# Kernel optimization log

Measured on AMD Instinct MI355X. Metric: run time of the kernel, lower is better.

The kernel has to match this reference:

```python
import jax, jax.numpy as jnp
import numpy as np

B, N = 64, 4096          # trees per batch, leaves per complete binary tree
V, S = 21, 50            # amino-acid vocab, grammar-symbol vocab
E, H = 64, 128           # embed_dim, hidden_dim


def setup_inputs() -> dict:
    key = jax.random.key(0)
    ks = jax.random.split(key, 16)

    def lin_w(k, din, dout):
        return (jax.random.normal(k, (dout, din), jnp.float32) / np.sqrt(din)).astype(jnp.float32)

    tokens = jax.random.randint(ks[0], (B, N), 0, V, dtype=jnp.int32)
    symbols = jax.random.randint(ks[1], (B, N - 1), 0, S, dtype=jnp.int32)

    emb = jax.random.normal(ks[2], (V, E), jnp.float32) * 0.02
    emb = emb.at[0].set(0.0)  # padding_idx=0
    sym_emb = jax.random.normal(ks[3], (S, E), jnp.float32) * 0.02

    return {
        "tokens": tokens, "symbols": symbols,
        "emb": emb, "sym_emb": sym_emb,
        "Wp": lin_w(ks[4], E, H), "bp": jnp.zeros((H,), jnp.float32),
        "Wi": lin_w(ks[5], H, H), "bi": jnp.zeros((H,), jnp.float32),
        "Ui": lin_w(ks[6], H, H),
        "Wf": lin_w(ks[7], H, H), "bf": jnp.zeros((H,), jnp.float32),
        "Uf": lin_w(ks[8], H, H),
        "Wo": lin_w(ks[9], H, H), "bo": jnp.zeros((H,), jnp.float32),
        "Uo": lin_w(ks[10], H, H),
        "Wu": lin_w(ks[11], H, H), "bu": jnp.zeros((H,), jnp.float32),
        "Uu": lin_w(ks[12], H, H),
        "Wout": lin_w(ks[13], H, H), "bout": jnp.zeros((H,), jnp.float32),
    }


def _encode(tokens, symbols, emb, sym_emb, Wp, bp, Wi, bi, Ui, Wf, bf, Uf,
            Wo, bo, Uo, Wu, bu, Uu, Wout, bout):
    emb = emb.at[0].set(0.0)  # padding row contributes nothing (and gets no grad)

    # Leaf nodes: amino-acid embedding -> input_proj, no children.
    x = emb[tokens] @ Wp.T + bp                      # [B, N, H]
    i = jax.nn.sigmoid(x @ Wi.T + bi)
    o = jax.nn.sigmoid(x @ Wo.T + bo)
    u = jnp.tanh(x @ Wu.T + bu)
    c = i * u                                        # [B, N, H]
    h = o * jnp.tanh(c)

    # Bottom-up over levels of the complete binary tree (Child-Sum Tree-LSTM).
    off, n = 0, N
    while n > 1:
        m = n // 2
        xs = sym_emb[symbols[:, off:off + m]] @ Wp.T + bp   # [B, m, H]
        hl, hr = h[:, 0::2], h[:, 1::2]
        cl, cr = c[:, 0::2], c[:, 1::2]
        ht = hl + hr                                         # h_tilde = sum_j h_j
        gi = jax.nn.sigmoid(xs @ Wi.T + bi + ht @ Ui.T)
        go = jax.nn.sigmoid(xs @ Wo.T + bo + ht @ Uo.T)
        gu = jnp.tanh(xs @ Wu.T + bu + ht @ Uu.T)
        fx = xs @ Wf.T + bf
        fl = jax.nn.sigmoid(fx + hl @ Uf.T)                  # per-child forget gates
        fr = jax.nn.sigmoid(fx + hr @ Uf.T)
        c = gi * gu + fl * cl + fr * cr
        h = go * jnp.tanh(c)
        off += m
        n = m

    root_h = h[:, 0]                                         # [B, H]
    return root_h @ Wout.T + bout                            # output_proj


def reference(tokens, symbols, emb, sym_emb, Wp, bp, Wi, bi, Ui, Wf, bf, Uf,
              Wo, bo, Uo, Wu, bu, Uu, Wout, bout):
    return _encode(tokens, symbols, emb, sym_emb, Wp, bp, Wi, bi, Ui, Wf, bf,
                   Uf, Wo, bo, Uo, Wu, bu, Uu, Wout, bout)
```

## Files before the change

### kernel.cpp

```cpp
#include <hip/hip_runtime.h>
#include <hip/hip_bf16.h>

typedef __attribute__((ext_vector_type(8))) short short8;
typedef __attribute__((ext_vector_type(4))) float f32x4;

static constexpr int B_ = 64;
static constexpr int N_ = 4096;
static constexpr int V_ = 21;
static constexpr int S_ = 50;
static constexpr int E_ = 64;
static constexpr int H_ = 128;
static constexpr int NPAIR = V_ * V_;
static constexpr int NTAB = NPAIR * S_;

__device__ __forceinline__ float rcp_(float x) { return __builtin_amdgcn_rcpf(x); }
__device__ __forceinline__ float sigm(float x) { return rcp_(1.0f + __expf(-x)); }
__device__ __forceinline__ float tanh_(float x) {
  float a = fabsf(x);
  float e = __expf(-2.0f * a);
  float t = (1.0f - e) * rcp_(1.0f + e);
  return x < 0.0f ? -t : t;
}
__device__ __forceinline__ unsigned short f2bf(float f) {
  __hip_bfloat16 b = __float2bfloat16(f);
  return *reinterpret_cast<unsigned short*>(&b);
}
__device__ __forceinline__ float bf2f(unsigned short u) {
  return __uint_as_float(((unsigned int)u) << 16);
}

struct Gates { float cv, hv; };
__device__ __forceinline__ Gates gate_combine(float4 sx,
    float i_p, float o_p, float u_p, float fl_p, float fr_p, float cl, float cr) {
  float gi = sigm(sx.x + i_p);
  float go = sigm(sx.y + o_p);
  float gu = tanh_(sx.z + u_p);
  float fl = sigm(sx.w + fl_p);
  float fr = sigm(sx.w + fr_p);
  float cv = fmaf(gi, gu, fmaf(fl, cl, fr * cr));
  Gates g; g.cv = cv; g.hv = go * tanh_(cv);
  return g;
}

__global__ void __launch_bounds__(512) k_pre0(
    const float* __restrict__ Ui, const float* __restrict__ Uo,
    const float* __restrict__ Uu, const float* __restrict__ Uf,
    const float* __restrict__ Wi, const float* __restrict__ Wo,
    const float* __restrict__ Wu, const float* __restrict__ Wf,
    const float* __restrict__ Wp, const float* __restrict__ Wout,
    unsigned short* __restrict__ Wfrag, float* __restrict__ Wt,
    float* __restrict__ Wxt, float* __restrict__ Wpt,
    float* __restrict__ Woutt) {
  __shared__ float Tt[32][129];
  int blk = blockIdx.x, t = threadIdx.x;
  if (blk < 16) {
    int idx = blk * 512 + t;
    int L = idx & 63;
    int K = (idx >> 6) & 3;
    int T = idx >> 8;
    int n = 16 * T + (L & 15);
    int k0 = 32 * K + ((L >> 4) << 3);
    int g = n >> 7, o = n & 127;
    const float* U = (g == 0) ? Ui : (g == 1) ? Uo : (g == 2) ? Uu : Uf;
    unsigned short out[8];
    #pragma unroll
    for (int j = 0; j < 8; ++j) out[j] = f2bf(U[o * 128 + k0 + j]);
    *(int4*)(Wfrag + (size_t)idx * 8) = *(int4*)out;
  } else if (blk < 48) {
    int job = blk - 16;
    int m = job >> 2, kt = job & 3;
    int k0 = kt * 32;
    const float* M = (m == 0) ? Ui : (m == 1) ? Uo : (m == 2) ? Uu : (m == 3) ? Uf
                   : (m == 4) ? Wi : (m == 5) ? Wo : (m == 6) ? Wu : Wf;
    float* D = (m < 4) ? Wt : Wxt;
    int g = m & 3;
    #pragma unroll
    for (int pass = 0; pass < 2; ++pass) {
      int o = (t >> 3) + 64 * pass;
      int kk = 4 * (t & 7);
      float4 v = *(const float4*)(M + o * 128 + k0 + kk);
      Tt[kk][o] = v.x; Tt[kk + 1][o] = v.y; Tt[kk + 2][o] = v.z; Tt[kk + 3][o] = v.w;
    }
    __syncthreads();
    #pragma unroll
    for (int pass = 0; pass < 8; ++pass) {
      int kk = pass * 4 + (t >> 7);
      int o = t & 127;
      D[(size_t)(k0 + kk) * 512 + g * 128 + o] = Tt[kk][o];
    }
  } else if (blk == 48) {
    for (int i = t; i < E_ * H_; i += 512) {
      int e = i >> 7, o = i & 127;
      Wpt[i] = Wp[o * E_ + e];
    }
  } else {
    for (int i = t; i < H_ * H_; i += 512) {
      int k = i >> 7, o = i & 127;
      Woutt[i] = Wout[o * H_ + k];
    }
  }
}

__global__ void __launch_bounds__(512) k_pre1(
    const float* __restrict__ emb, const float* __restrict__ sym_emb,
    const float* __restrict__ Wpt, const float* __restrict__ Wxt,
    const float* __restrict__ Wt,
    const float* __restrict__ bp, const float* __restrict__ bi,
    const float* __restrict__ bo, const float* __restrict__ bu,
    const float* __restrict__ bfv,
    unsigned short* __restrict__ leaf_h8, float* __restrict__ leaf_c,
    float* __restrict__ symx, float* __restrict__ P_leaf) {
  __shared__ float x[128];
  __shared__ float zs[512];
  __shared__ float hl[128];
  int blk = blockIdx.x, t = threadIdx.x;
  if (blk < V_) {
    int v = blk;
    if (t < 128) {
      float acc = bp[t];
      if (v != 0) {
        for (int e = 0; e < E_; ++e) acc = fmaf(emb[v * E_ + e], Wpt[e * 128 + t], acc);
      }
      x[t] = acc;
    }
    __syncthreads();
    if (t < 384) {
      int g = t >> 7;
      const float* bb = (g == 0) ? bi : (g == 1) ? bo : bu;
      float z = bb[t & 127];
      for (int k = 0; k < H_; ++k) z = fmaf(x[k], Wxt[k * 512 + t], z);
      zs[t] = z;
    }
    __syncthreads();
    if (t < 128) {
      float gi = sigm(zs[t]), go = sigm(zs[128 + t]), gu = tanh_(zs[256 + t]);
      float c = gi * gu;
      leaf_c[v * H_ + t] = c;
      unsigned short hb = f2bf(go * tanh_(c));
      leaf_h8[v * H_ + t] = hb;
      hl[t] = bf2f(hb);
    }
    __syncthreads();
    {
      float z = 0.f;
      for (int k = 0; k < H_; ++k) z = fmaf(hl[k], Wt[k * 512 + t], z);
      P_leaf[(size_t)v * 512 + t] = z;
    }
  } else {
    int s = blk - V_;
    if (t < 128) {
      float acc = bp[t];
      for (int e = 0; e < E_; ++e) acc = fmaf(sym_emb[s * E_ + e], Wpt[e * 128 + t], acc);
      x[t] = acc;
    }
    __syncthreads();
    {
      int g = t >> 7;
      const float* bb = (g == 0) ? bi : (g == 1) ? bo : (g == 2) ? bu : bfv;
      float z = bb[t & 127];
      for (int k = 0; k < H_; ++k) z = fmaf(x[k], Wxt[k * 512 + t], z);
      zs[t] = z;
    }
    __syncthreads();
    if (t < 128) {
      float4 v4 = make_float4(zs[t], zs[128 + t], zs[256 + t], zs[384 + t]);
      *(float4*)(symx + (size_t)s * 512 + t * 4) = v4;
    }
  }
}

__global__ void k_tabB(const float* __restrict__ P_leaf, const float* __restrict__ symx,
                       const float* __restrict__ leaf_c,
                       const int* __restrict__ tokens, const int* __restrict__ symbols,
                       unsigned short* __restrict__ tab_h8, float* __restrict__ tab_c,
                       int* __restrict__ idx1) {
  int blk = blockIdx.x, t = threadIdx.x;
  if (blk < NTAB / 2) {
    int row = blk * 2 + (t >> 7);
    int u = t & 127;
    int p = row / S_, s = row - p * S_;
    int tl = p / V_, tr = p - tl * V_;
    const float* Pl = P_leaf + (size_t)tl * 512;
    const float* Pr = P_leaf + (size_t)tr * 512;
    float4 sx = *(const float4*)(symx + (size_t)s * 512 + u * 4);
    Gates gt = gate_combine(sx,
        Pl[u] + Pr[u], Pl[128 + u] + Pr[128 + u], Pl[256 + u] + Pr[256 + u],
        Pl[384 + u], Pr[384 + u],
        leaf_c[tl * H_ + u], leaf_c[tr * H_ + u]);
    tab_c[(size_t)row * H_ + u] = gt.cv;
    tab_h8[(size_t)row * H_ + u] = f2bf(gt.hv);
  } else {
    int g = (blk - NTAB / 2) * 256 + t;
    int b = g >> 11, j = g & 2047;
    idx1[g] = (tokens[b * N_ + 2 * j] * V_ + tokens[b * N_ + 2 * j + 1]) * S_ + symbols[b * (N_ - 1) + j];
  }
}

__global__ void __launch_bounds__(512, 4) k_lvl23(
    const unsigned short* __restrict__ Wfrag, const float* __restrict__ symx,
    const int* __restrict__ symbols, const int* __restrict__ idx1,
    const unsigned short* __restrict__ gh8, const float* __restrict__ gc,
    unsigned short* __restrict__ h_out8, float* __restrict__ c_out) {
  __shared__ __align__(16) unsigned short Ag[32][136];
  __shared__ __align__(16) unsigned short Bh[16][136];
  __shared__ float Bc[16][132];
  int t = threadIdx.x;
  int w = t >> 6, L = t & 63, q = L >> 4, cL = L & 15;
  int cc = 16 * w + cL;
  int g0 = blockIdx.x * 16;
  int b = g0 >> 10;
  int j2 = g0 & 1023;
  const int* sym_b = symbols + (size_t)b * (N_ - 1);
  const int* gix = idx1 + 2 * g0;

  {
    int row = t >> 4, co = (t & 15) * 8;
    *(int4*)&Ag[row][co] = *(const int4*)(gh8 + (size_t)gix[row] * H_ + co);
  }
  __syncthreads();

  const short8* wf = (const short8*)Wfrag;
  {
    float clp[4], crp[4];
    int spre[4];
    #pragma unroll
    for (int it = 0; it < 4; ++it) {
      int n = 8 * (it >> 1) + 2 * q + (it & 1);
      clp[it] = gc[(size_t)gix[2 * n] * H_ + cc];
      crp[it] = gc[(size_t)gix[2 * n + 1] * H_ + cc];
      spre[it] = sym_b[2048 + j2 + n];
    }
    f32x4 acc[2][4];
    #pragma unroll
    for (int r = 0; r < 2; ++r)
      #pragma unroll
      for (int g = 0; g < 4; ++g) acc[r][g] = (f32x4){0.f, 0.f, 0.f, 0.f};
    #pragma unroll
    for (int K = 0; K < 4; ++K) {
      short8 bfr[4];
      #pragma unroll
      for (int g = 0; g < 4; ++g) bfr[g] = wf[(size_t)((w + 8 * g) * 4 + K) * 64 + L];
      short8 a0 = *(const short8*)&Ag[cL][K * 32 + q * 8];
      short8 a1 = *(const short8*)&Ag[16 + cL][K * 32 + q * 8];
      #pragma unroll
      for (int g = 0; g < 4; ++g) {
        acc[0][g] = __builtin_amdgcn_mfma_f32_16x16x32_bf16(a0, bfr[g], acc[0][g], 0, 0, 0);
        acc[1][g] = __builtin_amdgcn_mfma_f32_16x16x32_bf16(a1, bfr[g], acc[1][g], 0, 0, 0);
      }
    }
    #pragma unroll
    for (int r = 0; r < 2; ++r) {
      #pragma unroll
      for (int nd = 0; nd < 2; ++nd) {
        int it = r * 2 + nd;
        int n = 8 * r + 2 * q + nd;
        float4 sx = *(const float4*)(symx + (size_t)spre[it] * 512 + cc * 4);
        Gates gt = gate_combine(sx,
            acc[r][0][2 * nd] + acc[r][0][2 * nd + 1],
            acc[r][1][2 * nd] + acc[r][1][2 * nd + 1],
            acc[r][2][2 * nd] + acc[r][2][2 * nd + 1],
            acc[r][3][2 * nd], acc[r][3][2 * nd + 1], clp[it], crp[it]);
        Bc[n][cc] = gt.cv;
        Bh[n][cc] = f2bf(gt.hv);
      }
    }
  }
  __syncthreads();
  {
    int spre[2];
    #pragma unroll
    for (int nd = 0; nd < 2; ++nd) {
      int n = 2 * q + nd;
      spre[nd] = sym_b[3072 + (j2 >> 1) + n];
    }
    f32x4 acc[4];
    #pragma unroll
    for (int g = 0; g < 4; ++g) acc[g] = (f32x4){0.f, 0.f, 0.f, 0.f};
    #pragma unroll
    for (int K = 0; K < 4; ++K) {
      short8 bfr[4];
      #pragma unroll
      for (int g = 0; g < 4; ++g) bfr[g] = wf[(size_t)((w + 8 * g) * 4 + K) * 64 + L];
      short8 a0 = *(const short8*)&Bh[cL][K * 32 + q * 8];
      #pragma unroll
      for (int g = 0; g < 4; ++g)
        acc[g] = __builtin_amdgcn_mfma_f32_16x16x32_bf16(a0, bfr[g], acc[g], 0, 0, 0);
    }
    #pragma unroll
    for (int nd = 0; nd < 2; ++nd) {
      int n = 2 * q + nd;
      int G3 = (g0 >> 1) + n;
      float4 sx = *(const float4*)(symx + (size_t)spre[nd] * 512 + cc * 4);
      Gates gt = gate_combine(sx,
          acc[0][2 * nd] + acc[0][2 * nd + 1],
          acc[1][2 * nd] + acc[1][2 * nd + 1],
          acc[2][2 * nd] + acc[2][2 * nd + 1],
          acc[3][2 * nd], acc[3][2 * nd + 1],
          Bc[2 * n][cc], Bc[2 * n + 1][cc]);
      c_out[(size_t)G3 * H_ + cc] = gt.cv;
      h_out8[(size_t)G3 * H_ + cc] = f2bf(gt.hv);
    }
  }
}

__global__ void __launch_bounds__(512, 2) k_mid(
    const unsigned short* __restrict__ Wfrag, const float* __restrict__ symx,
    const int* __restrict__ symbols,
    const unsigned short* __restrict__ in_h8, const float* __restrict__ in_c,
    unsigned short* __restrict__ out_h8, float* __restrict__ out_c) {
  __shared__ __align__(16) unsigned short Ah0[64][136];
  __shared__ __align__(16) unsigned short Ah1[32][136];
  __shared__ float Cs0[64][128];
  __shared__ float Cs1[32][128];
  int t = threadIdx.x;
  int w = t >> 6, L = t & 63, q = L >> 4, cL = L & 15;
  int cc = 16 * w + cL;
  int blk = blockIdx.x;
  int b = blk >> 3, sub = blk & 7;
  size_t base3 = (size_t)blk * 64;

  #pragma unroll
  for (int i = 0; i < 2; ++i) {
    int fid = t + 512 * i;
    int row = fid >> 4, co = (fid & 15) * 8;
    *(int4*)&Ah0[row][co] = *(const int4*)(in_h8 + (base3 + row) * H_ + co);
  }
  #pragma unroll
  for (int i = 0; i < 4; ++i) {
    int fid = t + 512 * i;
    int row = fid >> 5, c4 = (fid & 31) << 2;
    *(float4*)&Cs0[row][c4] = *(const float4*)(in_c + (base3 + row) * H_ + c4);
  }
  __syncthreads();

  const short8* wf = (const short8*)Wfrag;
  int R = 64;
  #pragma unroll
  for (int lev = 0; lev < 6; ++lev) {
    const int l = 4 + lev;
    const int nodes = R >> 1;
    const int jb = b * (N_ - 1) + (N_ - (N_ >> (l - 1))) + ((sub * 32) >> lev);
    unsigned short (*Ard)[136] = (lev & 1) ? Ah1 : Ah0;
    unsigned short (*Awr)[136] = (lev & 1) ? Ah0 : Ah1;
    const float* crd = (lev & 1) ? &Cs1[0][0] : &Cs0[0][0];
    float* cwr = (lev & 1) ? &Cs0[0][0] : &Cs1[0][0];
    const int nchunk = (nodes + 15) >> 4;
    for (int c = 0; c < nchunk; ++c) {
      int spre[4];
      #pragma unroll
      for (int it = 0; it < 4; ++it) {
        int n = 16 * c + 8 * (it >> 1) + 2 * q + (it & 1);
        spre[it] = (n < nodes) ? symbols[jb + n] : 0;
      }
      f32x4 acc[2][4];
      #pragma unroll
      for (int r = 0; r < 2; ++r)
        #pragma unroll
        for (int g = 0; g < 4; ++g) acc[r][g] = (f32x4){0.f, 0.f, 0.f, 0.f};
      const bool useA1 = (2 * nodes - 32 * c) > 16;
      #pragma unroll
      for (int K = 0; K < 4; ++K) {
        short8 bfr[4];
        #pragma unroll
        for (int g = 0; g < 4; ++g) bfr[g] = wf[(size_t)((w + 8 * g) * 4 + K) * 64 + L];
        short8 a0 = *(const short8*)&Ard[32 * c + cL][K * 32 + q * 8];
        #pragma unroll
        for (int g = 0; g < 4; ++g)
          acc[0][g] = __builtin_amdgcn_mfma_f32_16x16x32_bf16(a0, bfr[g], acc[0][g], 0, 0, 0);
        if (useA1) {
          short8 a1 = *(const short8*)&Ard[32 * c + 16 + cL][K * 32 + q * 8];
          #pragma unroll
          for (int g = 0; g < 4; ++g)
            acc[1][g] = __builtin_amdgcn_mfma_f32_16x16x32_bf16(a1, bfr[g], acc[1][g], 0, 0, 0);
        }
      }
      #pragma unroll
      for (int r = 0; r < 2; ++r) {
        #pragma unroll
        for (int nd = 0; nd < 2; ++nd) {
          int it = r * 2 + nd;
          int n = 16 * c + 8 * r + 2 * q + nd;
          if (n < nodes) {
            float4 sx = *(const float4*)(symx + (size_t)spre[it] * 512 + cc * 4);
            Gates gt = gate_combine(sx,
                acc[r][0][2 * nd] + acc[r][0][2 * nd + 1],
                acc[r][1][2 * nd] + acc[r][1][2 * nd + 1],
                acc[r][2][2 * nd] + acc[r][2][2 * nd + 1],
                acc[r][3][2 * nd], acc[r][3][2 * nd + 1],
                crd[(size_t)(2 * n) * 128 + cc], crd[(size_t)(2 * n + 1) * 128 + cc]);
            if (lev == 5) {
              out_c[(size_t)blk * H_ + cc] = gt.cv;
              out_h8[(size_t)blk * H_ + cc] = f2bf(gt.hv);
            } else {
              cwr[(size_t)n * 128 + cc] = gt.cv;
              Awr[n][cc] = f2bf(gt.hv);
            }
          }
        }
      }
    }
    __syncthreads();
    R >>= 1;
  }
}

__global__ void __launch_bounds__(512, 2) k_fin(
    const unsigned short* __restrict__ Wfrag, const float* __restrict__ symx,
    const int* __restrict__ symbols,
    const unsigned short* __restrict__ in_h8, const float* __restrict__ in_c,
    const float* __restrict__ Woutt, const float* __restrict__ bout,
    float* __restrict__ out) {
  __shared__ __align__(16) unsigned short Ah0[8][136];
  __shared__ __align__(16) unsigned short Ah1[4][136];
  __shared__ float Cs0[8][128];
  __shared__ float Cs1[4][128];
  __shared__ float rootv[128];
  int t = threadIdx.x;
  int w = t >> 6, L = t & 63, q = L >> 4, cL = L & 15;
  int cc = 16 * w + cL;
  int b = blockIdx.x;

  if (t < 128) {
    int row = t >> 4, co = (t & 15) * 8;
    *(int4*)&Ah0[row][co] = *(const int4*)(in_h8 + (size_t)(b * 8 + row) * H_ + co);
  }
  if (t < 256) {
    int row = t >> 5, c4 = (t & 31) << 2;
    *(float4*)&Cs0[row][c4] = *(const float4*)(in_c + (size_t)(b * 8 + row) * H_ + c4);
  }
  __syncthreads();

  const short8* wf = (const short8*)Wfrag;
  int R = 8;
  #pragma unroll
  for (int lev = 0; lev < 3; ++lev) {
    const int l = 10 + lev;
    const int nodes = R >> 1;
    const int jb = b * (N_ - 1) + (N_ - (N_ >> (l - 1)));
    unsigned short (*Ard)[136] = (lev & 1) ? Ah1 : Ah0;
    unsigned short (*Awr)[136] = (lev & 1) ? Ah0 : Ah1;
    const float* crd = (lev & 1) ? &Cs1[0][0] : &Cs0[0][0];
    float* cwr = (lev & 1) ? &Cs0[0][0] : &Cs1[0][0];
    int spre[4];
    #pragma unroll
    for (int it = 0; it < 4; ++it) {
      int n = 8 * (it >> 1) + 2 * q + (it & 1);
      spre[it] = (n < nodes) ? symbols[jb + n] : 0;
    }
    f32x4 acc[4];
    #pragma unroll
    for (int g = 0; g < 4; ++g) acc[g] = (f32x4){0.f, 0.f, 0.f, 0.f};
    #pragma unroll
    for (int K = 0; K < 4; ++K) {
      short8 bfr[4];
      #pragma unroll
      for (int g = 0; g < 4; ++g) bfr[g] = wf[(size_t)((w + 8 * g) * 4 + K) * 64 + L];
      short8 a0 = *(const short8*)&Ard[cL & 7][K * 32 + q * 8];
      #pragma unroll
      for (int g = 0; g < 4; ++g)
        acc[g] = __builtin_amdgcn_mfma_f32_16x16x32_bf16(a0, bfr[g], acc[g], 0, 0, 0);
    }
    #pragma unroll
    for (int nd = 0; nd < 2; ++nd) {
      int it = nd;
      int n = 2 * q + nd;
      if (n < nodes) {
        float4 sx = *(const float4*)(symx + (size_t)spre[it] * 512 + cc * 4);
        Gates gt = gate_combine(sx,
            acc[0][2 * nd] + acc[0][2 * nd + 1],
            acc[1][2 * nd] + acc[1][2 * nd + 1],
            acc[2][2 * nd] + acc[2][2 * nd + 1],
            acc[3][2 * nd], acc[3][2 * nd + 1],
            crd[(size_t)(2 * n) * 128 + cc], crd[(size_t)(2 * n + 1) * 128 + cc]);
        if (lev == 2) {
          rootv[cc] = gt.hv;
        } else {
          cwr[(size_t)n * 128 + cc] = gt.cv;
          Awr[n][cc] = f2bf(gt.hv);
        }
      }
    }
    __syncthreads();
    R >>= 1;
  }
  if (t < 128) {
    float acc = bout[t];
    for (int k = 0; k < H_; ++k) acc = fmaf(rootv[k], Woutt[k * 128 + t], acc);
    out[(size_t)b * H_ + t] = acc;
  }
}

extern "C" void kernel_launch(void* const* d_in, const int* in_sizes, int n_in,
                              void* d_out, int out_size, void* d_ws, size_t ws_size,
                              hipStream_t stream) {
  const int* tokens    = (const int*)d_in[0];
  const int* symbols   = (const int*)d_in[1];
  const float* emb     = (const float*)d_in[2];
  const float* sym_emb = (const float*)d_in[3];
  const float* Wp  = (const float*)d_in[4];
  const float* bp  = (const float*)d_in[5];
  const float* Wi  = (const float*)d_in[6];
  const float* bi  = (const float*)d_in[7];
  const float* Ui  = (const float*)d_in[8];
  const float* Wf  = (const float*)d_in[9];
  const float* bf  = (const float*)d_in[10];
  const float* Uf  = (const float*)d_in[11];
  const float* Wo  = (const float*)d_in[12];
  const float* bo  = (const float*)d_in[13];
  const float* Uo  = (const float*)d_in[14];
  const float* Wu  = (const float*)d_in[15];
  const float* bu  = (const float*)d_in[16];
  const float* Uu  = (const float*)d_in[17];
  const float* Wout= (const float*)d_in[18];
  const float* bout= (const float*)d_in[19];

  char* ws = (char*)d_ws;
  unsigned short* Wfrag   = (unsigned short*)(ws);
  float*          Wt      = (float*)(ws + 131072);
  float*          Wxt     = (float*)(ws + 393216);
  float*          Wpt     = (float*)(ws + 655360);
  float*          Woutt   = (float*)(ws + 688128);
  unsigned short* leaf_h8 = (unsigned short*)(ws + 753664);
  float*          leaf_c  = (float*)(ws + 759040);
  float*          symx    = (float*)(ws + 769792);
  float*          P_leaf  = (float*)(ws + 872192);
  unsigned short* tab_h8  = (unsigned short*)(ws + 2001152UL);
  float*          tab_c   = (float*)(ws + 7645952UL);
  int*            idx1    = (int*)(ws + 18935552UL);
  unsigned short* L3h8    = (unsigned short*)(ws + 19459840UL);
  float*          L3c     = (float*)(ws + 27848448UL);
  unsigned short* L9h8    = (unsigned short*)(ws + 44625664UL);
  float*          L9c     = (float*)(ws + 44756736UL);

  k_pre0<<<50, 512, 0, stream>>>(Ui, Uo, Uu, Uf, Wi, Wo, Wu, Wf, Wp, Wout,
                                 Wfrag, Wt, Wxt, Wpt, Woutt);
  k_pre1<<<V_ + S_, 512, 0, stream>>>(emb, sym_emb, Wpt, Wxt, Wt,
                                      bp, bi, bo, bu, bf,
                                      leaf_h8, leaf_c, symx, P_leaf);
  k_tabB<<<NTAB / 2 + 512, 256, 0, stream>>>(P_leaf, symx, leaf_c, tokens, symbols,
                                             tab_h8, tab_c, idx1);
  k_lvl23<<<4096, 512, 0, stream>>>(Wfrag, symx, symbols, idx1, tab_h8, tab_c, L3h8, L3c);
  k_mid<<<512, 512, 0, stream>>>(Wfrag, symx, symbols, L3h8, L3c, L9h8, L9c);
  k_fin<<<B_, 512, 0, stream>>>(Wfrag, symx, symbols, L9h8, L9c, Woutt, bout,
                                (float*)d_out);
}
```

Baseline: 221.5 us.

## Compute first tree level on the fly instead of a precomputed lookup table

Drops the table kernel that precomputed level-1 node states for every (left token, right token, symbol) combination, about 22k rows. The gate math now runs inside k_lvl23 from the leaf projections and symbol projections, and the packed index build moves into k_pre0. This removes one kernel launch and the table writes and gather reads. In exchange it redoes the level-1 transcendental math per actual node, 128k nodes versus 22k table rows, and adds an extra shared-memory buffer to k_lvl23, which may lower occupancy.

```diff
diff --git a/kernel.cpp b/kernel.cpp
--- a/kernel.cpp
+++ b/kernel.cpp
@@ -10,8 +10,6 @@
 static constexpr int S_ = 50;
 static constexpr int E_ = 64;
 static constexpr int H_ = 128;
-static constexpr int NPAIR = V_ * V_;
-static constexpr int NTAB = NPAIR * S_;
 
 __device__ __forceinline__ float rcp_(float x) { return __builtin_amdgcn_rcpf(x); }
 __device__ __forceinline__ float sigm(float x) { return rcp_(1.0f + __expf(-x)); }
@@ -48,9 +46,10 @@
     const float* __restrict__ Wi, const float* __restrict__ Wo,
     const float* __restrict__ Wu, const float* __restrict__ Wf,
     const float* __restrict__ Wp, const float* __restrict__ Wout,
+    const int* __restrict__ tokens, const int* __restrict__ symbols,
     unsigned short* __restrict__ Wfrag, float* __restrict__ Wt,
     float* __restrict__ Wxt, float* __restrict__ Wpt,
-    float* __restrict__ Woutt) {
+    float* __restrict__ Woutt, int* __restrict__ idx1) {
   __shared__ float Tt[32][129];
   int blk = blockIdx.x, t = threadIdx.x;
   if (blk < 16) {
@@ -93,11 +92,18 @@
       int e = i >> 7, o = i & 127;
       Wpt[i] = Wp[o * E_ + e];
     }
-  } else {
+  } else if (blk == 49) {
     for (int i = t; i < H_ * H_; i += 512) {
       int k = i >> 7, o = i & 127;
       Woutt[i] = Wout[o * H_ + k];
     }
+  } else {
+    int g = (blk - 50) * 512 + t;
+    int b = g >> 11, j = g & 2047;
+    int tl = tokens[b * N_ + 2 * j];
+    int tr = tokens[b * N_ + 2 * j + 1];
+    int s = symbols[b * (N_ - 1) + j];
+    idx1[g] = tl | (tr << 8) | (s << 16);
   }
 }
 
@@ -108,8 +114,8 @@
     const float* __restrict__ bp, const float* __restrict__ bi,
     const float* __restrict__ bo, const float* __restrict__ bu,
     const float* __restrict__ bfv,
-    unsigned short* __restrict__ leaf_h8, float* __restrict__ leaf_c,
-    float* __restrict__ symx, float* __restrict__ P_leaf) {
+    float* __restrict__ leaf_c, float* __restrict__ symx,
+    float* __restrict__ P_leaf) {
   __shared__ float x[128];
   __shared__ float zs[512];
   __shared__ float hl[128];
@@ -137,7 +143,6 @@
       float c = gi * gu;
       leaf_c[v * H_ + t] = c;
       unsigned short hb = f2bf(go * tanh_(c));
-      leaf_h8[v * H_ + t] = hb;
       hl[t] = bf2f(hb);
     }
     __syncthreads();
@@ -169,39 +174,13 @@
   }
 }
 
-__global__ void k_tabB(const float* __restrict__ P_leaf, const float* __restrict__ symx,
-                       const float* __restrict__ leaf_c,
-                       const int* __restrict__ tokens, const int* __restrict__ symbols,
-                       unsigned short* __restrict__ tab_h8, float* __restrict__ tab_c,
-                       int* __restrict__ idx1) {
-  int blk = blockIdx.x, t = threadIdx.x;
-  if (blk < NTAB / 2) {
-    int row = blk * 2 + (t >> 7);
-    int u = t & 127;
-    int p = row / S_, s = row - p * S_;
-    int tl = p / V_, tr = p - tl * V_;
-    const float* Pl = P_leaf + (size_t)tl * 512;
-    const float* Pr = P_leaf + (size_t)tr * 512;
-    float4 sx = *(const float4*)(symx + (size_t)s * 512 + u * 4);
-    Gates gt = gate_combine(sx,
-        Pl[u] + Pr[u], Pl[128 + u] + Pr[128 + u], Pl[256 + u] + Pr[256 + u],
-        Pl[384 + u], Pr[384 + u],
-        leaf_c[tl * H_ + u], leaf_c[tr * H_ + u]);
-    tab_c[(size_t)row * H_ + u] = gt.cv;
-    tab_h8[(size_t)row * H_ + u] = f2bf(gt.hv);
-  } else {
-    int g = (blk - NTAB / 2) * 256 + t;
-    int b = g >> 11, j = g & 2047;
-    idx1[g] = (tokens[b * N_ + 2 * j] * V_ + tokens[b * N_ + 2 * j + 1]) * S_ + symbols[b * (N_ - 1) + j];
-  }
-}
-
 __global__ void __launch_bounds__(512, 4) k_lvl23(
     const unsigned short* __restrict__ Wfrag, const float* __restrict__ symx,
     const int* __restrict__ symbols, const int* __restrict__ idx1,
-    const unsigned short* __restrict__ gh8, const float* __restrict__ gc,
+    const float* __restrict__ P_leaf, const float* __restrict__ leaf_c,
     unsigned short* __restrict__ h_out8, float* __restrict__ c_out) {
   __shared__ __align__(16) unsigned short Ag[32][136];
+  __shared__ float C1[32][132];
   __shared__ __align__(16) unsigned short Bh[16][136];
   __shared__ float Bc[16][132];
   int t = threadIdx.x;
@@ -213,21 +192,30 @@
   const int* sym_b = symbols + (size_t)b * (N_ - 1);
   const int* gix = idx1 + 2 * g0;
 
-  {
-    int row = t >> 4, co = (t & 15) * 8;
-    *(int4*)&Ag[row][co] = *(const int4*)(gh8 + (size_t)gix[row] * H_ + co);
+  #pragma unroll 2
+  for (int p = 0; p < 8; ++p) {
+    int row = 4 * p + (t >> 7);
+    int u = t & 127;
+    int pk = gix[row];
+    int tl = pk & 255, tr = (pk >> 8) & 255, s = pk >> 16;
+    const float* Pl = P_leaf + (size_t)tl * 512;
+    const float* Pr = P_leaf + (size_t)tr * 512;
+    float4 sx = *(const float4*)(symx + (size_t)s * 512 + u * 4);
+    Gates gt = gate_combine(sx,
+        Pl[u] + Pr[u], Pl[128 + u] + Pr[128 + u], Pl[256 + u] + Pr[256 + u],
+        Pl[384 + u], Pr[384 + u],
+        leaf_c[tl * H_ + u], leaf_c[tr * H_ + u]);
+    C1[row][u] = gt.cv;
+    Ag[row][u] = f2bf(gt.hv);
   }
   __syncthreads();
 
   const short8* wf = (const short8*)Wfrag;
   {
-    float clp[4], crp[4];
     int spre[4];
     #pragma unroll
     for (int it = 0; it < 4; ++it) {
       int n = 8 * (it >> 1) + 2 * q + (it & 1);
-      clp[it] = gc[(size_t)gix[2 * n] * H_ + cc];
-      crp[it] = gc[(size_t)gix[2 * n + 1] * H_ + cc];
       spre[it] = sym_b[2048 + j2 + n];
     }
     f32x4 acc[2][4];
@@ -259,7 +247,8 @@
             acc[r][0][2 * nd] + acc[r][0][2 * nd + 1],
             acc[r][1][2 * nd] + acc[r][1][2 * nd + 1],
             acc[r][2][2 * nd] + acc[r][2][2 * nd + 1],
-            acc[r][3][2 * nd], acc[r][3][2 * nd + 1], clp[it], crp[it]);
+            acc[r][3][2 * nd], acc[r][3][2 * nd + 1],
+            C1[2 * n][cc], C1[2 * n + 1][cc]);
         Bc[n][cc] = gt.cv;
         Bh[n][cc] = f2bf(gt.hv);
       }
@@ -520,26 +509,23 @@
   float*          Wxt     = (float*)(ws + 393216);
   float*          Wpt     = (float*)(ws + 655360);
   float*          Woutt   = (float*)(ws + 688128);
-  unsigned short* leaf_h8 = (unsigned short*)(ws + 753664);
   float*          leaf_c  = (float*)(ws + 759040);
   float*          symx    = (float*)(ws + 769792);
   float*          P_leaf  = (float*)(ws + 872192);
-  unsigned short* tab_h8  = (unsigned short*)(ws + 2001152UL);
-  float*          tab_c   = (float*)(ws + 7645952UL);
   int*            idx1    = (int*)(ws + 18935552UL);
   unsigned short* L3h8    = (unsigned short*)(ws + 19459840UL);
   float*          L3c     = (float*)(ws + 27848448UL);
   unsigned short* L9h8    = (unsigned short*)(ws + 44625664UL);
   float*          L9c     = (float*)(ws + 44756736UL);
 
-  k_pre0<<<50, 512, 0, stream>>>(Ui, Uo, Uu, Uf, Wi, Wo, Wu, Wf, Wp, Wout,
-                                 Wfrag, Wt, Wxt, Wpt, Woutt);
+  k_pre0<<<306, 512, 0, stream>>>(Ui, Uo, Uu, Uf, Wi, Wo, Wu, Wf, Wp, Wout,
+                                  tokens, symbols,
+                                  Wfrag, Wt, Wxt, Wpt, Woutt, idx1);
   k_pre1<<<V_ + S_, 512, 0, stream>>>(emb, sym_emb, Wpt, Wxt, Wt,
                                       bp, bi, bo, bu, bf,
-                                      leaf_h8, leaf_c, symx, P_leaf);
-  k_tabB<<<NTAB / 2 + 512, 256, 0, stream>>>(P_leaf, symx, leaf_c, tokens, symbols,
-                                             tab_h8, tab_c, idx1);
-  k_lvl23<<<4096, 512, 0, stream>>>(Wfrag, symx, symbols, idx1, tab_h8, tab_c, L3h8, L3c);
+                                      leaf_c, symx, P_leaf);
+  k_lvl23<<<4096, 512, 0, stream>>>(Wfrag, symx, symbols, idx1, P_leaf, leaf_c,
+                                    L3h8, L3c);
   k_mid<<<512, 512, 0, stream>>>(Wfrag, symx, symbols, L3h8, L3c, L9h8, L9c);
   k_fin<<<B_, 512, 0, stream>>>(Wfrag, symx, symbols, L9h8, L9c, Woutt, bout,
                                 (float*)d_out);
```

Result: slower. 244.2 us (+10.3%).

## Make k_lvl23 persistent over 8 tiles with register-resident weights and prefetch

Applied to the files above, without the earlier changes.

k_lvl23 now launches 512 blocks, each looping over 8 consecutive tiles instead of one tile per block. The bf16 weight fragments are loaded into registers once per block and reused by both MFMA stages instead of being reloaded from global memory for each K step. Next-tile gather indices, symbols and the A-row h vector are prefetched while the current tile computes, and hand-written barriers replace __syncthreads. An unused leaf_h8 output is also removed. Holding 64 short8 weight registers raises register pressure, and the occupancy hint of 4 in the launch bounds is dropped.

```diff
diff --git a/kernel.cpp b/kernel.cpp
--- a/kernel.cpp
+++ b/kernel.cpp
@@ -40,6 +40,17 @@
   float cv = fmaf(gi, gu, fmaf(fl, cl, fr * cr));
   Gates g; g.cv = cv; g.hv = go * tanh_(cv);
   return g;
+}
+
+__device__ __forceinline__ void bar_lds() {
+  asm volatile("s_waitcnt lgkmcnt(0)" ::: "memory");
+  __builtin_amdgcn_s_barrier();
+  asm volatile("" ::: "memory");
+}
+__device__ __forceinline__ void bar_only() {
+  asm volatile("" ::: "memory");
+  __builtin_amdgcn_s_barrier();
+  asm volatile("" ::: "memory");
 }
 
 __global__ void __launch_bounds__(512) k_pre0(
@@ -108,8 +119,8 @@
     const float* __restrict__ bp, const float* __restrict__ bi,
     const float* __restrict__ bo, const float* __restrict__ bu,
     const float* __restrict__ bfv,
-    unsigned short* __restrict__ leaf_h8, float* __restrict__ leaf_c,
-    float* __restrict__ symx, float* __restrict__ P_leaf) {
+    float* __restrict__ leaf_c, float* __restrict__ symx,
+    float* __restrict__ P_leaf) {
   __shared__ float x[128];
   __shared__ float zs[512];
   __shared__ float hl[128];
@@ -137,7 +148,6 @@
       float c = gi * gu;
       leaf_c[v * H_ + t] = c;
       unsigned short hb = f2bf(go * tanh_(c));
-      leaf_h8[v * H_ + t] = hb;
       hl[t] = bf2f(hb);
     }
     __syncthreads();
@@ -196,7 +206,7 @@
   }
 }
 
-__global__ void __launch_bounds__(512, 4) k_lvl23(
+__global__ void __launch_bounds__(512) k_lvl23(
     const unsigned short* __restrict__ Wfrag, const float* __restrict__ symx,
     const int* __restrict__ symbols, const int* __restrict__ idx1,
     const unsigned short* __restrict__ gh8, const float* __restrict__ gc,
@@ -204,32 +214,72 @@
   __shared__ __align__(16) unsigned short Ag[32][136];
   __shared__ __align__(16) unsigned short Bh[16][136];
   __shared__ float Bc[16][132];
-  int t = threadIdx.x;
-  int w = t >> 6, L = t & 63, q = L >> 4, cL = L & 15;
-  int cc = 16 * w + cL;
-  int g0 = blockIdx.x * 16;
-  int b = g0 >> 10;
-  int j2 = g0 & 1023;
-  const int* sym_b = symbols + (size_t)b * (N_ - 1);
-  const int* gix = idx1 + 2 * g0;
-
+  const int t = threadIdx.x;
+  const int w = t >> 6, L = t & 63, q = L >> 4, cL = L & 15;
+  const int cc = 16 * w + cL;
+  const int rowA = t >> 4, coA = (t & 15) * 8;
+
+  const short8* wf = (const short8*)Wfrag;
+  short8 bfr[4][4];
+  #pragma unroll
+  for (int K = 0; K < 4; ++K)
+    #pragma unroll
+    for (int g = 0; g < 4; ++g)
+      bfr[g][K] = wf[(size_t)((w + 8 * g) * 4 + K) * 64 + L];
+
+  const int CH = 8;
+  const int t0 = blockIdx.x * CH;
+
+  int nn[4];
+  #pragma unroll
+  for (int it = 0; it < 4; ++it) nn[it] = 8 * (it >> 1) + 2 * q + (it & 1);
+
+  int gxr = idx1[t0 * 32 + rowA];
+  int4 agv = *(const int4*)(gh8 + (size_t)gxr * H_ + coA);
+  int g2l[4], g2r[4], sp1[4];
   {
-    int row = t >> 4, co = (t & 15) * 8;
-    *(int4*)&Ag[row][co] = *(const int4*)(gh8 + (size_t)gix[row] * H_ + co);
-  }
-  __syncthreads();
-
-  const short8* wf = (const short8*)Wfrag;
-  {
+    const int* sb = symbols + (size_t)(t0 >> 6) * (N_ - 1);
+    const int j20 = (t0 & 63) * 16;
+    #pragma unroll
+    for (int it = 0; it < 4; ++it) {
+      g2l[it] = idx1[t0 * 32 + 2 * nn[it]];
+      g2r[it] = idx1[t0 * 32 + 2 * nn[it] + 1];
+      sp1[it] = sb[2048 + j20 + nn[it]];
+    }
+  }
+
+  for (int k = 0; k < CH; ++k) {
+    const int tile = t0 + k;
+    const int j2 = (tile & 63) * 16;
+    const int* sb = symbols + (size_t)(tile >> 6) * (N_ - 1);
+
+    bar_only();
+    *(int4*)&Ag[rowA][coA] = agv;
+    bar_lds();
+
     float clp[4], crp[4];
-    int spre[4];
     #pragma unroll
     for (int it = 0; it < 4; ++it) {
-      int n = 8 * (it >> 1) + 2 * q + (it & 1);
-      clp[it] = gc[(size_t)gix[2 * n] * H_ + cc];
-      crp[it] = gc[(size_t)gix[2 * n + 1] * H_ + cc];
-      spre[it] = sym_b[2048 + j2 + n];
-    }
+      clp[it] = gc[(size_t)g2l[it] * H_ + cc];
+      crp[it] = gc[(size_t)g2r[it] * H_ + cc];
+    }
+    int gxr_n = 0, g2l_n[4], g2r_n[4], sp1_n[4];
+    if (k + 1 < CH) {
+      const int tn = tile + 1;
+      const int* sbn = symbols + (size_t)(tn >> 6) * (N_ - 1);
+      const int j2n = (tn & 63) * 16;
+      gxr_n = idx1[tn * 32 + rowA];
+      #pragma unroll
+      for (int it = 0; it < 4; ++it) {
+        g2l_n[it] = idx1[tn * 32 + 2 * nn[it]];
+        g2r_n[it] = idx1[tn * 32 + 2 * nn[it] + 1];
+        sp1_n[it] = sbn[2048 + j2n + nn[it]];
+      }
+    }
+    int sp2[2];
+    sp2[0] = sb[3072 + (j2 >> 1) + 2 * q];
+    sp2[1] = sb[3072 + (j2 >> 1) + 2 * q + 1];
+
     f32x4 acc[2][4];
     #pragma unroll
     for (int r = 0; r < 2; ++r)
@@ -237,24 +287,23 @@
       for (int g = 0; g < 4; ++g) acc[r][g] = (f32x4){0.f, 0.f, 0.f, 0.f};
     #pragma unroll
     for (int K = 0; K < 4; ++K) {
-      short8 bfr[4];
-      #pragma unroll
-      for (int g = 0; g < 4; ++g) bfr[g] = wf[(size_t)((w + 8 * g) * 4 + K) * 64 + L];
       short8 a0 = *(const short8*)&Ag[cL][K * 32 + q * 8];
       short8 a1 = *(const short8*)&Ag[16 + cL][K * 32 + q * 8];
       #pragma unroll
       for (int g = 0; g < 4; ++g) {
-        acc[0][g] = __builtin_amdgcn_mfma_f32_16x16x32_bf16(a0, bfr[g], acc[0][g], 0, 0, 0);
-        acc[1][g] = __builtin_amdgcn_mfma_f32_16x16x32_bf16(a1, bfr[g], acc[1][g], 0, 0, 0);
-      }
-    }
+        acc[0][g] = __builtin_amdgcn_mfma_f32_16x16x32_bf16(a0, bfr[g][K], acc[0][g], 0, 0, 0);
+        acc[1][g] = __builtin_amdgcn_mfma_f32_16x16x32_bf16(a1, bfr[g][K], acc[1][g], 0, 0, 0);
+      }
+    }
+    if (k + 1 < CH) agv = *(const int4*)(gh8 + (size_t)gxr_n * H_ + coA);
+
     #pragma unroll
     for (int r = 0; r < 2; ++r) {
       #pragma unroll
       for (int nd = 0; nd < 2; ++nd) {
         int it = r * 2 + nd;
         int n = 8 * r + 2 * q + nd;
-        float4 sx = *(const float4*)(symx + (size_t)spre[it] * 512 + cc * 4);
+        float4 sx = *(const float4*)(symx + (size_t)sp1[it] * 512 + cc * 4);
         Gates gt = gate_combine(sx,
             acc[r][0][2 * nd] + acc[r][0][2 * nd + 1],
             acc[r][1][2 * nd] + acc[r][1][2 * nd + 1],
@@ -264,41 +313,36 @@
         Bh[n][cc] = f2bf(gt.hv);
       }
     }
-  }
-  __syncthreads();
-  {
-    int spre[2];
+    bar_lds();
+
+    f32x4 acc2[4];
+    #pragma unroll
+    for (int g = 0; g < 4; ++g) acc2[g] = (f32x4){0.f, 0.f, 0.f, 0.f};
+    #pragma unroll
+    for (int K = 0; K < 4; ++K) {
+      short8 a0 = *(const short8*)&Bh[cL][K * 32 + q * 8];
+      #pragma unroll
+      for (int g = 0; g < 4; ++g)
+        acc2[g] = __builtin_amdgcn_mfma_f32_16x16x32_bf16(a0, bfr[g][K], acc2[g], 0, 0, 0);
+    }
     #pragma unroll
     for (int nd = 0; nd < 2; ++nd) {
       int n = 2 * q + nd;
-      spre[nd] = sym_b[3072 + (j2 >> 1) + n];
-    }
-    f32x4 acc[4];
-    #pragma unroll
-    for (int g = 0; g < 4; ++g) acc[g] = (f32x4){0.f, 0.f, 0.f, 0.f};
-    #pragma unroll
-    for (int K = 0; K < 4; ++K) {
-      short8 bfr[4];
-      #pragma unroll
-      for (int g = 0; g < 4; ++g) bfr[g] = wf[(size_t)((w + 8 * g) * 4 + K) * 64 + L];
-      short8 a0 = *(const short8*)&Bh[cL][K * 32 + q * 8];
-      #pragma unroll
-      for (int g = 0; g < 4; ++g)
-        acc[g] = __builtin_amdgcn_mfma_f32_16x16x32_bf16(a0, bfr[g], acc[g], 0, 0, 0);
-    }
-    #pragma unroll
-    for (int nd = 0; nd < 2; ++nd) {
-      int n = 2 * q + nd;
-      int G3 = (g0 >> 1) + n;
-      float4 sx = *(const float4*)(symx + (size_t)spre[nd] * 512 + cc * 4);
+      int G3 = tile * 8 + n;
+      float4 sx = *(const float4*)(symx + (size_t)sp2[nd] * 512 + cc * 4);
       Gates gt = gate_combine(sx,
-          acc[0][2 * nd] + acc[0][2 * nd + 1],
-          acc[1][2 * nd] + acc[1][2 * nd + 1],
-          acc[2][2 * nd] + acc[2][2 * nd + 1],
-          acc[3][2 * nd], acc[3][2 * nd + 1],
+          acc2[0][2 * nd] + acc2[0][2 * nd + 1],
+          acc2[1][2 * nd] + acc2[1][2 * nd + 1],
+          acc2[2][2 * nd] + acc2[2][2 * nd + 1],
+          acc2[3][2 * nd], acc2[3][2 * nd + 1],
           Bc[2 * n][cc], Bc[2 * n + 1][cc]);
       c_out[(size_t)G3 * H_ + cc] = gt.cv;
       h_out8[(size_t)G3 * H_ + cc] = f2bf(gt.hv);
+    }
+    gxr = gxr_n;
+    #pragma unroll
+    for (int it = 0; it < 4; ++it) {
+      g2l[it] = g2l_n[it]; g2r[it] = g2r_n[it]; sp1[it] = sp1_n[it];
     }
   }
 }
@@ -520,7 +564,6 @@
   float*          Wxt     = (float*)(ws + 393216);
   float*          Wpt     = (float*)(ws + 655360);
   float*          Woutt   = (float*)(ws + 688128);
-  unsigned short* leaf_h8 = (unsigned short*)(ws + 753664);
   float*          leaf_c  = (float*)(ws + 759040);
   float*          symx    = (float*)(ws + 769792);
   float*          P_leaf  = (float*)(ws + 872192);
@@ -536,10 +579,11 @@
                                  Wfrag, Wt, Wxt, Wpt, Woutt);
   k_pre1<<<V_ + S_, 512, 0, stream>>>(emb, sym_emb, Wpt, Wxt, Wt,
                                       bp, bi, bo, bu, bf,
-                                      leaf_h8, leaf_c, symx, P_leaf);
+                                      leaf_c, symx, P_leaf);
   k_tabB<<<NTAB / 2 + 512, 256, 0, stream>>>(P_leaf, symx, leaf_c, tokens, symbols,
                                              tab_h8, tab_c, idx1);
-  k_lvl23<<<4096, 512, 0, stream>>>(Wfrag, symx, symbols, idx1, tab_h8, tab_c, L3h8, L3c);
+  k_lvl23<<<512, 512, 0, stream>>>(Wfrag, symx, symbols, idx1, tab_h8, tab_c,
+                                   L3h8, L3c);
   k_mid<<<512, 512, 0, stream>>>(Wfrag, symx, symbols, L3h8, L3c, L9h8, L9c);
   k_fin<<<B_, 512, 0, stream>>>(Wfrag, symx, symbols, L9h8, L9c, Woutt, bout,
                                 (float*)d_out);
```

New measurement: 200.4 us. -9.5%, faster.
